# Performance work log

Measured on AMD Instinct MI355X. Metric: run time of the kernel, lower is better.

The kernel has to match this reference:

```python
import jax, jax.numpy as jnp
import numpy as np

N_NODES = 200000
N_EDGES = 6400000
IN_CH, HID, OUT_CH = 14, 16, 2


def gcn_conv(x, W, b, src, dst, n_nodes):
    """GCNConv with self-loops and symmetric normalization (PyG defaults).

    out[i] = sum_{j->i} d[i]^-1/2 d[j]^-1/2 (xW)[j] + d[i]^-1 (xW)[i] + b,
    where d = degree(A + I) computed on the target index.
    """
    h = x @ W  # [N, F_out]
    ones = jnp.ones((src.shape[0],), dtype=x.dtype)
    deg = jax.ops.segment_sum(ones, dst, num_segments=n_nodes) + 1.0  # +1 self-loop
    dinv = jax.lax.rsqrt(deg)  # [N]
    norm = dinv[src] * dinv[dst]  # [E]
    msg = h[src] * norm[:, None]  # [E, F_out] -- dominant memory traffic
    agg = jax.ops.segment_sum(msg, dst, num_segments=n_nodes)
    self_loop = h * (dinv * dinv)[:, None]
    return agg + self_loop + b


def setup_inputs() -> dict:
    key = jax.random.key(0)
    k1, k2, k3, k4, k5 = jax.random.split(key, 5)
    x = jax.random.normal(k1, (N_NODES, IN_CH), dtype=jnp.float32)
    edge_index = jax.random.randint(k2, (2, N_EDGES), 0, N_NODES, dtype=jnp.int64)
    edge_attr = jax.random.normal(k3, (N_EDGES, 1), dtype=jnp.float32)  # unused by GCNConv
    s = 1.0 / np.sqrt(IN_CH)
    W1 = jax.random.uniform(k4, (IN_CH, HID), jnp.float32, -s, s)
    b1 = jnp.zeros((HID,), jnp.float32)
    s2 = 1.0 / np.sqrt(HID)
    W2 = jax.random.uniform(k5, (HID, OUT_CH), jnp.float32, -s2, s2)
    b2 = jnp.zeros((OUT_CH,), jnp.float32)
    return {"x": x, "edge_index": edge_index, "edge_attr": edge_attr,
            "W1": W1, "b1": b1, "W2": W2, "b2": b2}


def reference(x, edge_index, edge_attr, W1, b1, W2, b2):
    src, dst = edge_index[0], edge_index[1]
    n = x.shape[0]
    h = jax.nn.relu(gcn_conv(x, W1, b1, src, dst, n))
    # F.dropout(training=self.training) is identity in eval mode
    out = gcn_conv(h, W2, b2, src, dst, n)
    return out
```

## Files before the change

kernel.cpp:

```cpp
#include <hip/hip_runtime.h>
#include <hip/hip_fp16.h>


constexpr int NN = 200000;
constexpr int NE = 6400000;
constexpr int IC = 14;
constexpr int HC = 16;
constexpr int OC = 2;

constexpr int NBK = 392;
constexpr int NSUB = 8;
constexpr int SCAP = 2816;
constexpr int NSEG = NSUB * NBK;
constexpr int CCAP = NSUB * SCAP;
constexpr int SPT = (SCAP + 1023) / 1024;
constexpr int TILE = 5120;
constexpr int BTH = 512;
constexpr int IPT = TILE / BTH;
constexpr int IPT2 = IPT / 2;
constexpr int NTILE = NE / TILE;
constexpr int OVFCAP = 65536;
constexpr int NM = NN / 32;
constexpr int GSTR = 16;

typedef unsigned long long ull;
typedef float f4v __attribute__((ext_vector_type(4)));

__device__ __forceinline__ int phase_of(unsigned src) {
    return src >= 100000u ? (src >= 150000u ? 3 : 2) : (src >= 50000u ? 1 : 0);
}

__device__ __forceinline__ int xcc_id() {
    int x;
    asm volatile("s_getreg_b32 %0, hwreg(HW_REG_XCC_ID)" : "=s"(x));
    return x & 7;
}

__device__ __forceinline__ void acc8(float* av, uint4 u) {
    float2 f0 = __half22float2(*(__half2*)&u.x);
    float2 f1 = __half22float2(*(__half2*)&u.y);
    float2 f2 = __half22float2(*(__half2*)&u.z);
    float2 f3 = __half22float2(*(__half2*)&u.w);
    av[0] += f0.x; av[1] += f0.y; av[2] += f1.x; av[3] += f1.y;
    av[4] += f2.x; av[5] += f2.y; av[6] += f3.x; av[7] += f3.y;
}

__global__ void k_init(int* __restrict__ gcur, const void* __restrict__ ei,
                       int* __restrict__ flag) {
    int i = blockIdx.x * blockDim.x + threadIdx.x;
    if (i < NSEG) gcur[i * GSTR] = i * SCAP;
    else if (i <= NSEG + 4) gcur[i * GSTR] = 0;
    if (i == 500) {
        const ull* p = (const ull*)ei;
        ull acc = 0ULL;
        for (int k = 0; k < 64; ++k) acc |= (p[k] >> 32);
        *flag = (acc == 0ULL) ? 1 : 0;
    }
}

__global__ __launch_bounds__(BTH, 6) void k_binA(const void* __restrict__ ei,
                                                 const int* __restrict__ flag,
                                                 int* __restrict__ gcur,
                                                 unsigned* __restrict__ binned,
                                                 ull* __restrict__ ovf) {
    __shared__ int hist[NBK];
    __shared__ int lofs[NBK];
    __shared__ int gofs[NBK];
    __shared__ int wsum[BTH / 64];
    __shared__ unsigned stage[TILE];

    int t = threadIdx.x;
    int fl = *flag;
    int tile0 = blockIdx.x * TILE;
    int segbase = xcc_id() * NBK;

    if (t < NBK) hist[t] = 0;
    __syncthreads();

    int dbuf[IPT], sbuf[IPT];
    const int* pw = (const int*)ei;
    if (fl) {
#pragma unroll
        for (int k = 0; k < IPT2; ++k) {
            int e = tile0 + k * (2 * BTH) + 2 * t;
            dbuf[2 * k] = pw[2 * (NE + e)];
            dbuf[2 * k + 1] = pw[2 * (NE + e) + 2];
            sbuf[2 * k] = pw[2 * e];
            sbuf[2 * k + 1] = pw[2 * e + 2];
        }
    } else {
#pragma unroll
        for (int k = 0; k < IPT2; ++k) {
            int e = tile0 + k * (2 * BTH) + 2 * t;
            uint2 dd = *(const uint2*)(pw + NE + e);
            uint2 ss = *(const uint2*)(pw + e);
            dbuf[2 * k] = (int)dd.x;
            dbuf[2 * k + 1] = (int)dd.y;
            sbuf[2 * k] = (int)ss.x;
            sbuf[2 * k + 1] = (int)ss.y;
        }
    }

    unsigned pk[IPT];
    unsigned ra[IPT];
#pragma unroll
    for (int k = 0; k < IPT; ++k) {
        int d = dbuf[k];
        int b = d >> 9;
        int r = atomicAdd(&hist[b], 1);
        pk[k] = ((unsigned)(d & 511) << 18) | (unsigned)sbuf[k];
        ra[k] = ((unsigned)r << 9) | (unsigned)b;
    }
    __syncthreads();

    int h0 = 0, h1 = 0, p = 0;
    if (t < NBK / 2) {
        h0 = hist[2 * t];
        h1 = hist[2 * t + 1];
        p = h0 + h1;
    }
    int lane = t & 63;
    int w = t >> 6;
    int incl = p;
#pragma unroll
    for (int off = 1; off < 64; off <<= 1) {
        int v = __shfl_up(incl, off, 64);
        if (lane >= off) incl += v;
    }
    if (lane == 63) wsum[w] = incl;
    __syncthreads();
    int wbase = 0;
#pragma unroll
    for (int ww = 0; ww < BTH / 64; ++ww) wbase += (ww < w) ? wsum[ww] : 0;
    int ex = wbase + incl - p;
    if (t < NBK / 2) {
        lofs[2 * t] = ex;
        lofs[2 * t + 1] = ex + h0;
    }
    if (t < NBK) gofs[t] = atomicAdd(&gcur[(segbase + t) * GSTR], hist[t]);
    __syncthreads();

#pragma unroll
    for (int k = 0; k < IPT; ++k) {
        int b = (int)(ra[k] & 511u);
        int r = (int)(ra[k] >> 9);
        stage[lofs[b] + r] = pk[k];
    }
    __syncthreads();

    for (int i = t; i < TILE; i += BTH) {
        int b = (i * 313) >> 12;
        if (b > NBK - 1) b = NBK - 1;
        while (b < NBK - 1 && lofs[b + 1] <= i) ++b;
        while (lofs[b] > i) --b;
        unsigned pack = stage[i];
        int seg = segbase + b;
        int dest = gofs[b] + (i - lofs[b]);
        if (dest < (seg + 1) * SCAP) {
            binned[dest] = pack;
        } else {
            int op = atomicAdd(&gcur[NSEG * GSTR], 1);
            if (op < OVFCAP) {
                int d = (b << 9) | (int)(pack >> 18);
                int s = (int)(pack & 0x3FFFF);
                ovf[op] = ((ull)d << 32) | (unsigned)s;
            }
        }
    }
}

__global__ __launch_bounds__(1024, 4) void k_sort(const int* __restrict__ gcur,
                                                  const unsigned* __restrict__ binned,
                                                  const ull* __restrict__ ovf,
                                                  const float* __restrict__ x,
                                                  unsigned* __restrict__ csr,
                                                  float* __restrict__ dinv,
                                                  int* __restrict__ rsg,
                                                  unsigned* __restrict__ spl,
                                                  __half* __restrict__ xph) {
    __shared__ int cnt[2048];
    __shared__ int excl[2048];
    __shared__ int wsum[16];
    __shared__ int nseg[NSUB];
    __shared__ float sdv[512];
    __shared__ unsigned stage[CCAP];
    int b = blockIdx.x;
    int t = threadIdx.x;
    cnt[t] = 0;
    cnt[t + 1024] = 0;
    if (t < NSUB) {
        int seg = t * NBK + b;
        nseg[t] = min(gcur[seg * GSTR] - seg * SCAP, SCAP);
    }
    __syncthreads();
    int nov = min(gcur[NSEG * GSTR], OVFCAP);

    unsigned srcv[NSUB * SPT];
    unsigned rkv[NSUB * SPT];
#pragma unroll
    for (int s = 0; s < NSUB; ++s) {
        int n = nseg[s];
        int sb = (s * NBK + b) * SCAP;
#pragma unroll
        for (int k = 0; k < SPT; ++k) {
            int i = k * 1024 + t;
            rkv[s * SPT + k] = 0xFFFFFFFFu;
            if (i < n) {
                unsigned pack = binned[sb + i];
                unsigned src = pack & 0x3FFFFu;
                int key = ((int)(pack >> 18) << 2) | phase_of(src);
                int r = atomicAdd(&cnt[key], 1);
                srcv[s * SPT + k] = src;
                rkv[s * SPT + k] = ((unsigned)r << 11) | (unsigned)key;
            }
        }
    }
    __syncthreads();

    int h0 = cnt[2 * t];
    int h1 = cnt[2 * t + 1];
    int p = h0 + h1;
    int lane = t & 63;
    int w = t >> 6;
    int incl = p;
#pragma unroll
    for (int off = 1; off < 64; off <<= 1) {
        int v = __shfl_up(incl, off, 64);
        if (lane >= off) incl += v;
    }
    if (lane == 63) wsum[w] = incl;
    __syncthreads();
    int wbase = 0;
#pragma unroll
    for (int ww = 0; ww < 16; ++ww) wbase += (ww < w) ? wsum[ww] : 0;
    int ex = wbase + incl - p;
    excl[2 * t] = ex;
    excl[2 * t + 1] = ex + h0;
    __syncthreads();

#pragma unroll
    for (int c = 0; c < NSUB * SPT; ++c) {
        unsigned rk = rkv[c];
        if (rk != 0xFFFFFFFFu) {
            int key = (int)(rk & 0x7FFu);
            int r = (int)(rk >> 11);
            stage[excl[key] + r] = srcv[c];
        }
    }

    if (t < 512) {
        int g = (b << 9) + t;
        if (g < NN) {
            int c0 = cnt[4 * t];
            int c1 = cnt[4 * t + 1];
            int c2 = cnt[4 * t + 2];
            int c3 = cnt[4 * t + 3];
            int extra = 0;
            for (int k = 0; k < nov; ++k) extra += ((int)(ovf[k] >> 32) == g);
            float dv = rsqrtf((float)(c0 + c1 + c2 + c3 + extra) + 1.0f);
            dinv[g] = dv;
            sdv[t] = dv;
            rsg[g] = b * CCAP + excl[4 * t];
            spl[g] = (unsigned)c0 | ((unsigned)c1 << 8) |
                     ((unsigned)c2 << 16) | ((unsigned)c3 << 24);
        }
    }
    __syncthreads();

    int total = excl[2047] + cnt[2047];
    int tot4 = (total + 3) >> 2;
    const uint4* st4 = (const uint4*)stage;
    uint4* csr4 = (uint4*)(csr + (size_t)b * CCAP);
#pragma unroll
    for (int k = 0; k < (CCAP / 4 + 1023) / 1024; ++k) {
        int i4 = k * 1024 + t;
        if (i4 < tot4) csr4[i4] = st4[i4];
    }

    {
        int n512 = t >> 1;
        int g = (b << 9) + n512;
        if (g < NN) {
            float dv = sdv[n512];
            int cb = 8 * (t & 1);
            const float* xr = x + (size_t)g * IC;
            float v[8];
#pragma unroll
            for (int c = 0; c < 8; c += 2) {
                int ch = cb + c;
                if (ch + 1 < IC) {
                    float2 xx = *(const float2*)(xr + ch);
                    v[c] = dv * xx.x;
                    v[c + 1] = dv * xx.y;
                } else {
                    v[c] = 0.0f;
                    v[c + 1] = 0.0f;
                }
            }
            __half2 p0 = __floats2half2_rn(v[0], v[1]);
            __half2 p1 = __floats2half2_rn(v[2], v[3]);
            __half2 p2 = __floats2half2_rn(v[4], v[5]);
            __half2 p3 = __floats2half2_rn(v[6], v[7]);
            uint4 pk4;
            pk4.x = *(unsigned*)&p0;
            pk4.y = *(unsigned*)&p1;
            pk4.z = *(unsigned*)&p2;
            pk4.w = *(unsigned*)&p3;
            *(uint4*)(xph + (size_t)g * 16 + cb) = pk4;
        }
    }
}

__global__ __launch_bounds__(256) void k_agg1f(const int* __restrict__ rsg,
                                               const unsigned* __restrict__ spl,
                                               const unsigned* __restrict__ csr,
                                               const __half* __restrict__ xph,
                                               const int* __restrict__ gcur,
                                               const ull* __restrict__ ovf,
                                               const float* __restrict__ dinv,
                                               const float* __restrict__ W1,
                                               const float* __restrict__ b1,
                                               const float* __restrict__ W2,
                                               const float* __restrict__ b2,
                                               float2* __restrict__ h2bp,
                                               float2* __restrict__ selfout) {
    __shared__ float sW1[IC * HC];
    __shared__ float sb1[HC];
    __shared__ float sW2[HC * OC];
    __shared__ float sb2[OC];
    __shared__ float sAgg[32][17];
    int t = threadIdx.x;
    if (t < IC * HC) sW1[t] = W1[t];
    if (t < HC) sb1[t] = b1[t];
    if (t < HC * OC) sW2[t] = W2[t];
    if (t < OC) sb2[t] = b2[t];

    int g = t >> 3;
    int h = t & 7;
    int qc = h & 1;
    int eh = h >> 1;
    int i = blockIdx.x * 32 + g;
    unsigned sp = spl[i];
    int tot = (int)(sp & 255u) + (int)((sp >> 8) & 255u) +
              (int)((sp >> 16) & 255u) + (int)(sp >> 24);
    int beg = rsg[i];
    int end = beg + tot;

    float av[8];
#pragma unroll
    for (int c = 0; c < 8; ++c) av[c] = 0.0f;
    int j = beg + eh;
    int s0 = (j < end) ? (int)csr[j] : -1;
    int s1 = (j + 4 < end) ? (int)csr[j + 4] : -1;
    while (j < end) {
        int jn = j + 8;
        int n0 = (jn < end) ? (int)csr[jn] : -1;
        int n1 = (jn + 4 < end) ? (int)csr[jn + 4] : -1;
        uint4 u0 = *(const uint4*)(xph + (size_t)s0 * 16 + 8 * qc);
        acc8(av, u0);
        if (s1 >= 0) {
            uint4 u1 = *(const uint4*)(xph + (size_t)s1 * 16 + 8 * qc);
            acc8(av, u1);
        }
        s0 = n0;
        s1 = n1;
        j = jn;
    }

    if (eh == 0) {
        uint4 us = *(const uint4*)(xph + (size_t)i * 16 + 8 * qc);
        acc8(av, us);
    }
#pragma unroll
    for (int c = 0; c < 8; ++c) av[c] += __shfl_xor(av[c], 2);
#pragma unroll
    for (int c = 0; c < 8; ++c) av[c] += __shfl_xor(av[c], 4);

    float dv = dinv[i];
    if (eh == 0) {
        int nov = min(gcur[NSEG * GSTR], OVFCAP);
        for (int k = 0; k < nov; ++k) {
            ull e = ovf[k];
            if ((int)(e >> 32) == i) {
                int s = (int)(e & 0xFFFFFFFFu);
#pragma unroll
                for (int c = 0; c < 8; ++c)
                    av[c] += __half2float(xph[(size_t)s * 16 + 8 * qc + c]);
            }
        }
#pragma unroll
        for (int c = 0; c < 8; ++c) sAgg[g][8 * qc + c] = dv * av[c];
    }
    __syncthreads();

    int l8 = t & 7;
    float o0 = 0.0f, o1 = 0.0f;
#pragma unroll
    for (int f2 = 0; f2 < 2; ++f2) {
        int f = 2 * l8 + f2;
        float a = sb1[f];
#pragma unroll
        for (int c = 0; c < IC; ++c) a = fmaf(sAgg[g][c], sW1[c * HC + f], a);
        a = fmaxf(a, 0.0f);
        o0 = fmaf(a, sW2[f * OC + 0], o0);
        o1 = fmaf(a, sW2[f * OC + 1], o1);
    }
    o0 += __shfl_xor(o0, 1);
    o1 += __shfl_xor(o1, 1);
    o0 += __shfl_xor(o0, 2);
    o1 += __shfl_xor(o1, 2);
    o0 += __shfl_xor(o0, 4);
    o1 += __shfl_xor(o1, 4);
    if (l8 == 0) {
        h2bp[i] = make_float2(o0 * dv, o1 * dv);
        selfout[i] = make_float2(o0 * dv * dv + sb2[0], o1 * dv * dv + sb2[1]);
    }
}

__global__ __launch_bounds__(256) void k_agg2(const int* __restrict__ rsg,
                                              const unsigned* __restrict__ spl,
                                              const unsigned* __restrict__ csr,
                                              const int* __restrict__ gcur,
                                              const ull* __restrict__ ovf,
                                              const float* __restrict__ dinv,
                                              const float2* __restrict__ h2bp,
                                              const float2* __restrict__ selfout,
                                              float2* __restrict__ out) {
    int tt = blockIdx.x * 256 + threadIdx.x;
    int i = tt >> 3;
    int h = tt & 7;
    if (i >= NN) return;
    unsigned sp = spl[i];
    int tot = (int)(sp & 255u) + (int)((sp >> 8) & 255u) +
              (int)((sp >> 16) & 255u) + (int)(sp >> 24);
    int beg = rsg[i];
    int end = beg + tot;
    float ax = 0.0f, ay = 0.0f;
    int j = beg + h;
    int s0 = (j < end) ? (int)csr[j] : -1;
    int s1 = (j + 8 < end) ? (int)csr[j + 8] : -1;
    while (j < end) {
        int jn = j + 16;
        int n0 = (jn < end) ? (int)csr[jn] : -1;
        int n1 = (jn + 8 < end) ? (int)csr[jn + 8] : -1;
        float2 h0 = h2bp[s0];
        ax += h0.x;
        ay += h0.y;
        if (s1 >= 0) {
            float2 h1 = h2bp[s1];
            ax += h1.x;
            ay += h1.y;
        }
        s0 = n0;
        s1 = n1;
        j = jn;
    }
    ax += __shfl_xor(ax, 1);
    ay += __shfl_xor(ay, 1);
    ax += __shfl_xor(ax, 2);
    ay += __shfl_xor(ay, 2);
    ax += __shfl_xor(ax, 4);
    ay += __shfl_xor(ay, 4);
    if (h == 0) {
        int nov = min(gcur[NSEG * GSTR], OVFCAP);
        for (int k = 0; k < nov; ++k) {
            ull e = ovf[k];
            if ((int)(e >> 32) == i) {
                float2 hh = h2bp[(int)(e & 0xFFFFFFFFu)];
                ax += hh.x;
                ay += hh.y;
            }
        }
        float dv = dinv[i];
        float2 so = selfout[i];
        out[i] = make_float2(so.x + dv * ax, so.y + dv * ay);
    }
}

extern "C" void kernel_launch(void* const* d_in, const int* in_sizes, int n_in,
                              void* d_out, int out_size, void* d_ws, size_t ws_size,
                              hipStream_t stream) {
    const float* x = (const float*)d_in[0];
    const void* ei = d_in[1];
    const float* W1 = (const float*)d_in[3];
    const float* b1 = (const float*)d_in[4];
    const float* W2 = (const float*)d_in[5];
    const float* b2 = (const float*)d_in[6];
    float* out = (float*)d_out;

    ull* ovf = (ull*)d_ws;
    int* gcur = (int*)(ovf + OVFCAP);
    int* flag = gcur + (NSEG + 5) * GSTR;
    int* rsg = flag + 4;
    unsigned* spl = (unsigned*)(rsg + NN);
    float* dinv = (float*)(spl + NN);
    __half* xph = (__half*)(dinv + NN);
    float2* h2bp = (float2*)(xph + (size_t)NN * 16);
    float2* selfout = h2bp + NN;
    unsigned* binned = (unsigned*)(selfout + NN);
    unsigned* csr = binned + (size_t)NSEG * SCAP;

    k_init<<<(NSEG + 5 + 255) / 256, 256, 0, stream>>>(gcur, ei, flag);
    k_binA<<<NTILE, BTH, 0, stream>>>(ei, flag, gcur, binned, ovf);
    k_sort<<<NBK, 1024, 0, stream>>>(gcur, binned, ovf, x, csr, dinv, rsg, spl, xph);
    k_agg1f<<<NM, 256, 0, stream>>>(rsg, spl, csr, xph, gcur, ovf, dinv,
                                    W1, b1, W2, b2, h2bp, selfout);
    k_agg2<<<(NN * 8 + 255) / 256, 256, 0, stream>>>(rsg, spl, csr, gcur, ovf, dinv,
                                                     h2bp, selfout, (float2*)out);
}
```

Measured before the change: 270.3 us.

## Split half-precision features into two planes and aggregate each in separate passes

The 16-channel fp16 feature array is split into two 8-channel planes, and layer-1 aggregation becomes two kernels. Each kernel gathers only one plane, so its gather working set is halved (200k×16 B) and more likely to stay in cache. The first pass writes partial sums to scratch that reuses the binned buffer, and the second pass combines them with the self-loop, overflow edges and the MLP. The cost is an extra launch, reading the CSR index array twice, and a round trip of partial sums through memory.

```diff
diff --git a/kernel.cpp b/kernel.cpp
--- a/kernel.cpp
+++ b/kernel.cpp
@@ -177,7 +177,8 @@
                                                   float* __restrict__ dinv,
                                                   int* __restrict__ rsg,
                                                   unsigned* __restrict__ spl,
-                                                  __half* __restrict__ xph) {
+                                                  __half* __restrict__ xph0,
+                                                  __half* __restrict__ xph1) {
     __shared__ int cnt[2048];
     __shared__ int excl[2048];
     __shared__ int wsum[16];
@@ -282,7 +283,8 @@
         int g = (b << 9) + n512;
         if (g < NN) {
             float dv = sdv[n512];
-            int cb = 8 * (t & 1);
+            int pl = t & 1;
+            int cb = 8 * pl;
             const float* xr = x + (size_t)g * IC;
             float v[8];
 #pragma unroll
@@ -306,15 +308,68 @@
             pk4.y = *(unsigned*)&p1;
             pk4.z = *(unsigned*)&p2;
             pk4.w = *(unsigned*)&p3;
-            *(uint4*)(xph + (size_t)g * 16 + cb) = pk4;
-        }
-    }
-}
-
-__global__ __launch_bounds__(256) void k_agg1f(const int* __restrict__ rsg,
+            __half* dst = (pl ? xph1 : xph0) + (size_t)g * 8;
+            *(uint4*)dst = pk4;
+        }
+    }
+}
+
+__global__ __launch_bounds__(256) void k_agg1h(const int* __restrict__ rsg,
                                                const unsigned* __restrict__ spl,
                                                const unsigned* __restrict__ csr,
-                                               const __half* __restrict__ xph,
+                                               const __half* __restrict__ xp0,
+                                               float* __restrict__ agg0) {
+    int t = threadIdx.x;
+    int g = t >> 3;
+    int h = t & 7;
+    int i = blockIdx.x * 32 + g;
+    unsigned sp = spl[i];
+    int tot = (int)(sp & 255u) + (int)((sp >> 8) & 255u) +
+              (int)((sp >> 16) & 255u) + (int)(sp >> 24);
+    int beg = rsg[i];
+    int end = beg + tot;
+
+    float av[8];
+#pragma unroll
+    for (int c = 0; c < 8; ++c) av[c] = 0.0f;
+    int j = beg + h;
+    int s0 = (j < end) ? (int)csr[j] : -1;
+    int s1 = (j + 8 < end) ? (int)csr[j + 8] : -1;
+    while (j < end) {
+        int jn = j + 16;
+        int n0 = (jn < end) ? (int)csr[jn] : -1;
+        int n1 = (jn + 8 < end) ? (int)csr[jn + 8] : -1;
+        uint4 u0 = *(const uint4*)(xp0 + (size_t)s0 * 8);
+        acc8(av, u0);
+        if (s1 >= 0) {
+            uint4 u1 = *(const uint4*)(xp0 + (size_t)s1 * 8);
+            acc8(av, u1);
+        }
+        s0 = n0;
+        s1 = n1;
+        j = jn;
+    }
+#pragma unroll
+    for (int c = 0; c < 8; ++c) av[c] += __shfl_xor(av[c], 1);
+#pragma unroll
+    for (int c = 0; c < 8; ++c) av[c] += __shfl_xor(av[c], 2);
+#pragma unroll
+    for (int c = 0; c < 8; ++c) av[c] += __shfl_xor(av[c], 4);
+    if (h == 0) {
+        f4v r0 = {av[0], av[1], av[2], av[3]};
+        __builtin_nontemporal_store(r0, (f4v*)(agg0 + (size_t)i * 8));
+    } else if (h == 1) {
+        f4v r1 = {av[4], av[5], av[6], av[7]};
+        __builtin_nontemporal_store(r1, (f4v*)(agg0 + (size_t)i * 8 + 4));
+    }
+}
+
+__global__ __launch_bounds__(256) void k_agg1n(const int* __restrict__ rsg,
+                                               const unsigned* __restrict__ spl,
+                                               const unsigned* __restrict__ csr,
+                                               const __half* __restrict__ xp0,
+                                               const __half* __restrict__ xp1,
+                                               const float* __restrict__ agg0,
                                                const int* __restrict__ gcur,
                                                const ull* __restrict__ ovf,
                                                const float* __restrict__ dinv,
@@ -337,8 +392,6 @@
 
     int g = t >> 3;
     int h = t & 7;
-    int qc = h & 1;
-    int eh = h >> 1;
     int i = blockIdx.x * 32 + g;
     unsigned sp = spl[i];
     int tot = (int)(sp & 255u) + (int)((sp >> 8) & 255u) +
@@ -349,47 +402,58 @@
     float av[8];
 #pragma unroll
     for (int c = 0; c < 8; ++c) av[c] = 0.0f;
-    int j = beg + eh;
+    int j = beg + h;
     int s0 = (j < end) ? (int)csr[j] : -1;
-    int s1 = (j + 4 < end) ? (int)csr[j + 4] : -1;
+    int s1 = (j + 8 < end) ? (int)csr[j + 8] : -1;
     while (j < end) {
-        int jn = j + 8;
+        int jn = j + 16;
         int n0 = (jn < end) ? (int)csr[jn] : -1;
-        int n1 = (jn + 4 < end) ? (int)csr[jn + 4] : -1;
-        uint4 u0 = *(const uint4*)(xph + (size_t)s0 * 16 + 8 * qc);
+        int n1 = (jn + 8 < end) ? (int)csr[jn + 8] : -1;
+        uint4 u0 = *(const uint4*)(xp1 + (size_t)s0 * 8);
         acc8(av, u0);
         if (s1 >= 0) {
-            uint4 u1 = *(const uint4*)(xph + (size_t)s1 * 16 + 8 * qc);
+            uint4 u1 = *(const uint4*)(xp1 + (size_t)s1 * 8);
             acc8(av, u1);
         }
         s0 = n0;
         s1 = n1;
         j = jn;
     }
-
-    if (eh == 0) {
-        uint4 us = *(const uint4*)(xph + (size_t)i * 16 + 8 * qc);
-        acc8(av, us);
-    }
+#pragma unroll
+    for (int c = 0; c < 8; ++c) av[c] += __shfl_xor(av[c], 1);
 #pragma unroll
     for (int c = 0; c < 8; ++c) av[c] += __shfl_xor(av[c], 2);
 #pragma unroll
     for (int c = 0; c < 8; ++c) av[c] += __shfl_xor(av[c], 4);
 
     float dv = dinv[i];
-    if (eh == 0) {
+    if (h == 0) {
+        uint4 us1 = *(const uint4*)(xp1 + (size_t)i * 8);
+        acc8(av, us1);
+        float a0[8];
+        f4v p0 = __builtin_nontemporal_load((const f4v*)(agg0 + (size_t)i * 8));
+        f4v p1 = __builtin_nontemporal_load((const f4v*)(agg0 + (size_t)i * 8 + 4));
+        a0[0] = p0.x; a0[1] = p0.y; a0[2] = p0.z; a0[3] = p0.w;
+        a0[4] = p1.x; a0[5] = p1.y; a0[6] = p1.z; a0[7] = p1.w;
+        uint4 us0 = *(const uint4*)(xp0 + (size_t)i * 8);
+        acc8(a0, us0);
         int nov = min(gcur[NSEG * GSTR], OVFCAP);
         for (int k = 0; k < nov; ++k) {
             ull e = ovf[k];
             if ((int)(e >> 32) == i) {
                 int s = (int)(e & 0xFFFFFFFFu);
 #pragma unroll
-                for (int c = 0; c < 8; ++c)
-                    av[c] += __half2float(xph[(size_t)s * 16 + 8 * qc + c]);
+                for (int c = 0; c < 8; ++c) {
+                    a0[c] += __half2float(xp0[(size_t)s * 8 + c]);
+                    av[c] += __half2float(xp1[(size_t)s * 8 + c]);
+                }
             }
         }
 #pragma unroll
-        for (int c = 0; c < 8; ++c) sAgg[g][8 * qc + c] = dv * av[c];
+        for (int c = 0; c < 8; ++c) {
+            sAgg[g][c] = dv * a0[c];
+            sAgg[g][8 + c] = dv * av[c];
+        }
     }
     __syncthreads();
 
@@ -494,17 +558,21 @@
     int* rsg = flag + 4;
     unsigned* spl = (unsigned*)(rsg + NN);
     float* dinv = (float*)(spl + NN);
-    __half* xph = (__half*)(dinv + NN);
-    float2* h2bp = (float2*)(xph + (size_t)NN * 16);
+    __half* xph0 = (__half*)(dinv + NN);
+    __half* xph1 = xph0 + (size_t)NN * 8;
+    float2* h2bp = (float2*)(xph1 + (size_t)NN * 8);
     float2* selfout = h2bp + NN;
     unsigned* binned = (unsigned*)(selfout + NN);
+    float* agg0 = (float*)binned;
     unsigned* csr = binned + (size_t)NSEG * SCAP;
 
     k_init<<<(NSEG + 5 + 255) / 256, 256, 0, stream>>>(gcur, ei, flag);
     k_binA<<<NTILE, BTH, 0, stream>>>(ei, flag, gcur, binned, ovf);
-    k_sort<<<NBK, 1024, 0, stream>>>(gcur, binned, ovf, x, csr, dinv, rsg, spl, xph);
-    k_agg1f<<<NM, 256, 0, stream>>>(rsg, spl, csr, xph, gcur, ovf, dinv,
-                                    W1, b1, W2, b2, h2bp, selfout);
+    k_sort<<<NBK, 1024, 0, stream>>>(gcur, binned, ovf, x, csr, dinv, rsg, spl,
+                                     xph0, xph1);
+    k_agg1h<<<NM, 256, 0, stream>>>(rsg, spl, csr, xph0, agg0);
+    k_agg1n<<<NM, 256, 0, stream>>>(rsg, spl, csr, xph0, xph1, agg0, gcur, ovf,
+                                    dinv, W1, b1, W2, b2, h2bp, selfout);
     k_agg2<<<(NN * 8 + 255) / 256, 256, 0, stream>>>(rsg, spl, csr, gcur, ovf, dinv,
                                                      h2bp, selfout, (float2*)out);
 }
```

After: 282.0 us. 4.3% more time.
